# Kernel tuning notes

Measured on AMD Instinct MI355X. Metric: run time of the kernel, lower is better.

Reference implementation:

```python
import jax, jax.numpy as jnp
import numpy as np

NUM_CLASSES = 5
DIM = 512
NUM_HEADS = 8
B, N = 8, 256


def setup_inputs() -> dict:
    key = jax.random.key(0)
    ks = jax.random.split(key, 7)
    s = 1.0 / np.sqrt(DIM)
    return {
        "x": jax.random.normal(ks[0], (B, N, DIM), dtype=jnp.float32),
        "anchors": jax.random.normal(ks[1], (NUM_CLASSES, N, DIM), dtype=jnp.float32),
        "weights": jax.random.uniform(ks[2], (B, NUM_HEADS, NUM_CLASSES), dtype=jnp.float32),
        "qk_w": jax.random.normal(ks[3], (DIM, DIM), dtype=jnp.float32) * s,
        "v_w": jax.random.normal(ks[4], (DIM, DIM), dtype=jnp.float32) * s,
        "proj_w": jax.random.normal(ks[5], (DIM, DIM), dtype=jnp.float32) * s,
        "proj_b": jnp.zeros((DIM,), dtype=jnp.float32),
    }


def reference(x, anchors, weights, qk_w, v_w, proj_w, proj_b):
    Bx, Nx, C = x.shape
    H = NUM_HEADS
    hd = C // H
    scale = hd ** (-0.5)

    # v: [B, H, N, hd]
    v = (x @ v_w.T).reshape(Bx, Nx, H, hd).transpose(0, 2, 1, 3)
    # q: [B, H, N, hd]; k: [cls, H, N, hd] (shared qk projection)
    q = (x @ qk_w.T).reshape(Bx, Nx, H, hd).transpose(0, 2, 1, 3)
    k = (anchors @ qk_w.T).reshape(NUM_CLASSES, Nx, H, hd).transpose(0, 2, 1, 3)

    # a0: [B, cls, H, N, N]
    a0 = jnp.einsum("bhnd,chmd->bchnm", q, k) * scale
    left = jax.nn.relu(-a0)                         # relu of negative branch
    right = jax.nn.relu(jnp.swapaxes(a0, -2, -1))   # relu of transposed positive branch
    # second large NxN matmul, then softmax over dim=-2 (columns)
    attn = jax.nn.softmax(left @ right, axis=-2)    # [B, cls, H, N, N]

    # class-weighted combine: weights [B, H, cls] -> tmp [B, H, N, N]
    tmp = jnp.einsum("bhc,bchnm->bhnm", weights, attn)

    # (tmp @ v): [B, H, N, hd]; torch reshapes directly to (B, N, C) without permute
    out = (tmp @ v).reshape(Bx, Nx, C)
    out = out @ proj_w.T + proj_b
    return (out, a0)
```

## Files before the change

### kernel.cpp

```cpp
#include <hip/hip_runtime.h>
#include <hip/hip_fp16.h>
#include <cstdint>

#define BB 8
#define NN 256
#define NC 5
#define NH 8
#define DIM 512
#define HD 64

typedef _Float16 half_t;
typedef _Float16 h8 __attribute__((ext_vector_type(8)));
typedef _Float16 h4 __attribute__((ext_vector_type(4)));
typedef float f4 __attribute__((ext_vector_type(4)));
typedef uint32_t u4v __attribute__((ext_vector_type(4)));

__device__ __forceinline__ f4 mfma16(h8 a, h8 b, f4 c) {
  return __builtin_amdgcn_mfma_f32_16x16x32_f16(a, b, c, 0, 0, 0);
}

static __device__ const h8 HZERO = {(_Float16)0, (_Float16)0, (_Float16)0, (_Float16)0,
                                    (_Float16)0, (_Float16)0, (_Float16)0, (_Float16)0};

__device__ __forceinline__ h8 relu_pos_h8(h8 x) {
#if __has_builtin(__builtin_elementwise_max)
  return __builtin_elementwise_max(x, HZERO);
#else
  u4v u = __builtin_bit_cast(u4v, x);
  const u4v k1 = {0x00010001u, 0x00010001u, 0x00010001u, 0x00010001u};
  u4v s = (u >> 15) & k1;
  u4v m = (s << 16) - s;
  u = u & ~m;
  return __builtin_bit_cast(h8, u);
#endif
}

__device__ __forceinline__ h8 relu_neg_h8(h8 x) {
#if __has_builtin(__builtin_elementwise_max)
  return __builtin_elementwise_max(-x, HZERO);
#else
  u4v u = __builtin_bit_cast(u4v, x);
  const u4v k1 = {0x00010001u, 0x00010001u, 0x00010001u, 0x00010001u};
  const u4v ks = {0x80008000u, 0x80008000u, 0x80008000u, 0x80008000u};
  u4v s = (u >> 15) & k1;
  u4v m = (s << 16) - s;
  u = (u ^ ks) & m;
  return __builtin_bit_cast(h8, u);
#endif
}

__device__ __forceinline__ void barrier_lds() {
  __builtin_amdgcn_sched_barrier(0);
  asm volatile("s_waitcnt lgkmcnt(0)" ::: "memory");
  __builtin_amdgcn_s_barrier();
  asm volatile("" ::: "memory");
  __builtin_amdgcn_sched_barrier(0);
}

__global__ __launch_bounds__(256) void cvt_all(const float* __restrict__ x,
                                               const float* __restrict__ anchors,
                                               const float* __restrict__ qk_w,
                                               const float* __restrict__ v_w,
                                               const float* __restrict__ proj_w,
                                               half_t* __restrict__ x_h,
                                               half_t* __restrict__ anc_h,
                                               half_t* __restrict__ qk_h,
                                               half_t* __restrict__ v_wh,
                                               half_t* __restrict__ pw_h) {
  int i = blockIdx.x * 256 + threadIdx.x;
  const float* src;
  half_t* dst;
  int off;
  if (i < 262144)      { src = x;       dst = x_h;   off = i; }
  else if (i < 425984) { src = anchors; dst = anc_h; off = i - 262144; }
  else if (i < 491520) { src = qk_w;    dst = qk_h;  off = i - 425984; }
  else if (i < 557056) { src = v_w;     dst = v_wh;  off = i - 491520; }
  else                 { src = proj_w;  dst = pw_h;  off = i - 557056; }
  float4 v = ((const float4*)src)[off];
  h4 o;
  o[0] = (_Float16)v.x; o[1] = (_Float16)v.y; o[2] = (_Float16)v.z; o[3] = (_Float16)v.w;
  ((h4*)dst)[off] = o;
}

__global__ __launch_bounds__(256) void proj_all(const half_t* __restrict__ x_h,
                                                const half_t* __restrict__ anc_h,
                                                const half_t* __restrict__ qk_h,
                                                const half_t* __restrict__ v_wh,
                                                half_t* __restrict__ q_h,
                                                half_t* __restrict__ k_h,
                                                half_t* __restrict__ vT) {
  const int bx = blockIdx.x, by = blockIdx.y;
  const int tid = threadIdx.x;
  const int w = tid >> 6, lane = tid & 63;
  const int lr = lane & 15, lk = (lane >> 4) * 8, lg = lane >> 4;

  const half_t* A;
  const half_t* W;
  int mode, rt0;
  if (bx < 32)      { A = x_h;   W = qk_h; mode = 0; rt0 = bx * 64; }
  else if (bx < 52) { A = anc_h; W = qk_h; mode = 1; rt0 = (bx - 32) * 64; }
  else              { A = x_h;   W = v_wh; mode = 2; rt0 = (bx - 52) * 64; }

  const int row0 = rt0 + w * 16;
  const int col0 = by * 64;
  const f4 fz = {0.f, 0.f, 0.f, 0.f};
  f4 acc[4] = {fz, fz, fz, fz};
  const half_t* arow = A + (size_t)(row0 + lr) * DIM;

  if (mode != 2) {
    for (int k0 = 0; k0 < DIM; k0 += 32) {
      h8 a = *(const h8*)(arow + k0 + lk);
#pragma unroll
      for (int ct = 0; ct < 4; ++ct) {
        h8 b = *(const h8*)(W + (size_t)(col0 + ct * 16 + lr) * DIM + k0 + lk);
        acc[ct] = mfma16(a, b, acc[ct]);
      }
    }
    half_t* out = (mode == 0) ? q_h : k_h;
#pragma unroll
    for (int ct = 0; ct < 4; ++ct) {
      int col = col0 + ct * 16 + lr;
#pragma unroll
      for (int r = 0; r < 4; ++r) {
        int row = row0 + lg * 4 + r;
        out[(size_t)row * DIM + col] = (half_t)acc[ct][r];
      }
    }
  } else {
    for (int k0 = 0; k0 < DIM; k0 += 32) {
      h8 a = *(const h8*)(arow + k0 + lk);
#pragma unroll
      for (int ct = 0; ct < 4; ++ct) {
        h8 b = *(const h8*)(W + (size_t)(col0 + ct * 16 + lr) * DIM + k0 + lk);
        acc[ct] = mfma16(b, a, acc[ct]);
      }
    }
    const int xrow = row0 + lr;
#pragma unroll
    for (int ct = 0; ct < 4; ++ct) {
#pragma unroll
      for (int r = 0; r < 4; ++r) {
        int col = col0 + ct * 16 + lg * 4 + r;
        vT[(size_t)col * (BB * NN) + xrow] = (half_t)acc[ct][r];
      }
    }
  }
}

__global__ __launch_bounds__(1024, 4) void fused_attn5(const half_t* __restrict__ q_h,
                                                       const half_t* __restrict__ k_h,
                                                       const half_t* __restrict__ vT,
                                                       const float* __restrict__ weights,
                                                       float* __restrict__ a0_base,
                                                       half_t* __restrict__ U4) {
  extern __shared__ char smem[];
  half_t* a0s = (half_t*)smem;
  half_t* kst = (half_t*)(smem + 65536);
  half_t* vst = kst;
  half_t* wbuf = (half_t*)(smem + 98304);
  float2* scr = (float2*)(smem + 118784);
  float2* scr2 = (float2*)(smem + 135168);

  const int id = blockIdx.x;
  const int b = id / 80;
  const int rem = id % 80;
  const int c = rem / 16;
  const int h = (rem >> 1) & 7;
  const int q = rem & 1;

  const int tid = threadIdx.x;
  const int w = tid >> 6, lane = tid & 63;
  const int lr = lane & 15, lk = (lane >> 4) * 8, lg = lane >> 4;
  const int n0 = w * 16;

  const half_t* qb = q_h + (size_t)(b * NN) * DIM + h * HD;
  const half_t* kb = k_h + (size_t)(c * NN) * DIM + h * HD;
  const half_t* vTb = vT + (size_t)(h * HD) * (BB * NN) + b * NN;
  float* a0out = a0_base + (size_t)((b * NC + c) * NH + h) * (NN * NN);
  const float wgt = weights[(b * NH + h) * NC + c];

  const f4 fz = {0.f, 0.f, 0.f, 0.f};

  h8 qf0 = *(const h8*)(qb + (size_t)(n0 + lr) * DIM + lk);
  h8 qf1 = *(const h8*)(qb + (size_t)(n0 + lr) * DIM + 32 + lk);

#pragma unroll
  for (int pass = 0; pass < 2; ++pass) {
    int slot = pass * 1024 + tid;
    int row = slot >> 3, k8 = (slot & 7) * 8;
    h8 val = *(const h8*)(kb + (size_t)row * DIM + k8);
    *(h8*)(kst + ((row * 64 + k8) ^ ((row & 7) << 3))) = val;
  }
  barrier_lds();

  half_t* Lb = wbuf + w * 640;
  h8 La[8];
  const bool myhalf = ((w >> 3) == q);
  const int rl = (w & 7) * 16 + lr;
#pragma unroll
  for (int mt = 0; mt < 16; ++mt) {
    const int krow = mt * 16 + lr;
    h8 kf0 = *(const h8*)(kst + ((krow * 64 + lk) ^ ((krow & 7) << 3)));
    h8 kf1 = *(const h8*)(kst + ((krow * 64 + 32 + lk) ^ ((krow & 7) << 3)));
    f4 acc = mfma16(kf0, qf0, fz);
    acc = mfma16(kf1, qf1, acc);
    f4 v0;
    h4 hv;
#pragma unroll
    for (int r = 0; r < 4; ++r) {
      v0[r] = acc[r] * 0.125f;
      hv[r] = (_Float16)v0[r];
    }
    *(h4*)(Lb + lr * 40 + (mt & 1) * 16 + lg * 4) = hv;
    if (myhalf) {
      *(f4*)(a0out + (size_t)(n0 + lr) * NN + mt * 16 + lg * 4) = v0;
      *(h4*)(a0s + ((rl * 256 + mt * 16 + lg * 4) ^ ((rl & 7) << 3))) = hv;
    }
    if (mt & 1) {
      h8 raw = *(const h8*)(Lb + lr * 40 + lg * 8);
      La[mt >> 1] = relu_neg_h8(raw);
    }
  }
  barrier_lds();

  {
    int d = tid >> 4, m8 = (tid & 15) * 8;
    h8 val = *(const h8*)(vTb + (size_t)d * (BB * NN) + q * 128 + m8);
    *(h8*)(vst + ((d * 128 + m8) ^ ((d & 7) << 4))) = val;
  }

  f4 sacc[8];
#pragma unroll
  for (int ct = 0; ct < 8; ++ct) sacc[ct] = fz;
#pragma unroll
  for (int kc = 0; kc < 8; ++kc) {
#pragma unroll
    for (int ct = 0; ct < 8; ++ct) {
      const int rr = ct * 16 + lr;
      h8 R = relu_pos_h8(*(const h8*)(a0s + ((rr * 256 + kc * 32 + lk) ^ ((rr & 7) << 3))));
      sacc[ct] = mfma16(La[kc], R, sacc[ct]);
    }
  }

  float mw[8];
#pragma unroll
  for (int ct = 0; ct < 8; ++ct) {
    float v = 0.f;
#pragma unroll
    for (int r = 0; r < 4; ++r) v = fmaxf(v, sacc[ct][r]);
    v = fmaxf(v, __shfl_xor(v, 16, 64));
    v = fmaxf(v, __shfl_xor(v, 32, 64));
    mw[ct] = v;
    float s = 0.f;
#pragma unroll
    for (int r = 0; r < 4; ++r) {
      float e = __expf(sacc[ct][r] - v);
      sacc[ct][r] = e;
      s += e;
    }
    s += __shfl_xor(s, 16, 64);
    s += __shfl_xor(s, 32, 64);
    if (lane < 16) {
      float2 t;
      t.x = v;
      t.y = s;
      scr[w * 128 + ct * 16 + lr] = t;
    }
  }
  barrier_lds();

  if (tid < 128) {
    float gm = 0.f;
#pragma unroll
    for (int ww = 0; ww < 16; ++ww) gm = fmaxf(gm, scr[ww * 128 + tid].x);
    float sg = 0.f;
#pragma unroll
    for (int ww = 0; ww < 16; ++ww) {
      float2 t = scr[ww * 128 + tid];
      sg += t.y * __expf(t.x - gm);
    }
    float2 r;
    r.x = gm;
    r.y = sg;
    scr2[tid] = r;
  }
  barrier_lds();

  float fac[8];
#pragma unroll
  for (int ct = 0; ct < 8; ++ct) {
    float2 t = scr2[ct * 16 + lr];
    fac[ct] = __expf(mw[ct] - t.x) * wgt / t.y;
  }

  half_t* pbw = wbuf + w * 640;
  f4 uacc[4] = {fz, fz, fz, fz};
#pragma unroll
  for (int pan = 0; pan < 4; ++pan) {
#pragma unroll
    for (int ctl = 0; ctl < 2; ++ctl) {
      const int ct = pan * 2 + ctl;
      h4 hv;
#pragma unroll
      for (int r = 0; r < 4; ++r) hv[r] = (_Float16)(sacc[ct][r] * fac[ct]);
      *(h4*)(pbw + (ctl * 16 + lr) * 20 + lg * 4) = hv;
    }
    h8 pf;
#pragma unroll
    for (int e = 0; e < 8; ++e) pf[e] = pbw[(lg * 8 + e) * 20 + lr];
#pragma unroll
    for (int dt = 0; dt < 4; ++dt) {
      const int dr = dt * 16 + lr;
      h8 vf = *(const h8*)(vst + ((dr * 128 + pan * 32 + lk) ^ ((dr & 7) << 4)));
      uacc[dt] = mfma16(vf, pf, uacc[dt]);
    }
  }

  half_t* U4b = U4 + (size_t)(((b * NC + c) * NH + h) * 2 + q) * (NN * HD);
#pragma unroll
  for (int dt = 0; dt < 4; ++dt) {
    h4 hv;
#pragma unroll
    for (int r = 0; r < 4; ++r) hv[r] = (_Float16)uacc[dt][r];
    *(h4*)(U4b + (size_t)(n0 + lr) * HD + dt * 16 + lg * 4) = hv;
  }
}

__global__ __launch_bounds__(256) void reduce_u(const half_t* __restrict__ U4,
                                                half_t* __restrict__ out_head) {
  int t = blockIdx.x * 256 + threadIdx.x;
  int bh = t >> 11;
  int e = (t & 2047) * 8;
  int b = bh >> 3, h = bh & 7;
  float acc[8] = {0.f, 0.f, 0.f, 0.f, 0.f, 0.f, 0.f, 0.f};
#pragma unroll
  for (int c = 0; c < NC; ++c)
#pragma unroll
    for (int qq = 0; qq < 2; ++qq) {
      h8 u = *(const h8*)(U4 + (size_t)(((b * NC + c) * NH + h) * 2 + qq) * (NN * HD) + e);
#pragma unroll
      for (int j = 0; j < 8; ++j) acc[j] += (float)u[j];
    }
  h8 o;
#pragma unroll
  for (int j = 0; j < 8; ++j) o[j] = (_Float16)acc[j];
  *(h8*)(out_head + (size_t)bh * (NN * HD) + e) = o;
}

__global__ __launch_bounds__(256) void out_proj(const half_t* __restrict__ out_head,
                                                const half_t* __restrict__ pw_h,
                                                const float* __restrict__ pb,
                                                float* __restrict__ out0) {
  const int tid = threadIdx.x;
  const int w = tid >> 6, lane = tid & 63;
  const int lr = lane & 15, lk = (lane >> 4) * 8, lg = lane >> 4;
  const int row0 = blockIdx.x * 64 + w * 16;
  const int col0 = blockIdx.y * 64;
  const int r_ = row0 + lr;
  const int b = r_ >> 8, i = r_ & 255;
  const int hh = i >> 5;
  const f4 fz = {0.f, 0.f, 0.f, 0.f};
  f4 acc[4] = {fz, fz, fz, fz};
  for (int k0 = 0; k0 < DIM; k0 += 32) {
    const int k = k0 + lk;
    const int n = ((i & 31) << 3) | (k >> 6);
    const int d = k & 63;
    h8 a = *(const h8*)(out_head + (size_t)((b * NH + hh) * NN + n) * HD + d);
#pragma unroll
    for (int ct = 0; ct < 4; ++ct) {
      h8 bf = *(const h8*)(pw_h + (size_t)(col0 + ct * 16 + lr) * DIM + k0 + lk);
      acc[ct] = mfma16(a, bf, acc[ct]);
    }
  }
#pragma unroll
  for (int ct = 0; ct < 4; ++ct) {
    int col = col0 + ct * 16 + lr;
    float bias = pb[col];
#pragma unroll
    for (int r = 0; r < 4; ++r) {
      int row = row0 + lg * 4 + r;
      out0[(size_t)row * DIM + col] = acc[ct][r] + bias;
    }
  }
}

extern "C" void kernel_launch(void* const* d_in, const int* in_sizes, int n_in,
                              void* d_out, int out_size, void* d_ws, size_t ws_size,
                              hipStream_t stream) {
  const float* x = (const float*)d_in[0];
  const float* anchors = (const float*)d_in[1];
  const float* weights = (const float*)d_in[2];
  const float* qk_w = (const float*)d_in[3];
  const float* v_w = (const float*)d_in[4];
  const float* proj_w = (const float*)d_in[5];
  const float* proj_b = (const float*)d_in[6];

  float* out0 = (float*)d_out;
  float* a0_out = out0 + (size_t)BB * NN * DIM;

  char* ws = (char*)d_ws;
  const size_t MB = 1024 * 1024;
  half_t* x_h   = (half_t*)(ws);
  half_t* anc_h = (half_t*)(ws + 2 * MB);
  half_t* qk_h  = (half_t*)(ws + 3407872);
  half_t* v_wh  = (half_t*)(ws + 3932160);
  half_t* U4    = (half_t*)(ws);
  half_t* pw_h     = (half_t*)(ws + 20 * MB);
  half_t* q_h      = (half_t*)(ws + 20 * MB + 524288);
  half_t* k_h      = (half_t*)(ws + 22 * MB + 524288);
  half_t* vT       = (half_t*)(ws + 24 * MB);
  half_t* out_head = (half_t*)(ws + 26 * MB);

  cvt_all<<<dim3(2432), 256, 0, stream>>>(x, anchors, qk_w, v_w, proj_w,
                                          x_h, anc_h, qk_h, v_wh, pw_h);

  proj_all<<<dim3(84, 8), 256, 0, stream>>>(x_h, anc_h, qk_h, v_wh, q_h, k_h, vT);

  const size_t lds_bytes = 65536 + 32768 + 20480 + 16384 + 1024;
  fused_attn5<<<dim3(BB * NC * NH * 2), 1024, lds_bytes, stream>>>(q_h, k_h, vT, weights,
                                                                   a0_out, U4);

  reduce_u<<<dim3(512), 256, 0, stream>>>(U4, out_head);

  out_proj<<<dim3(32, 8), 256, 0, stream>>>(out_head, pw_h, proj_b, out0);

  (void)in_sizes; (void)n_in; (void)out_size; (void)ws_size;
}
```

Measured before the change: 116.0 us.

## Compute full 256x256 a0 tile per block and split second matmul 2D across waves

```diff
diff --git a/kernel.cpp b/kernel.cpp
--- a/kernel.cpp
+++ b/kernel.cpp
@@ -147,7 +147,7 @@
   }
 }
 
-__global__ __launch_bounds__(1024, 4) void fused_attn5(const half_t* __restrict__ q_h,
+__global__ __launch_bounds__(1024, 4) void fused_attn8(const half_t* __restrict__ q_h,
                                                        const half_t* __restrict__ k_h,
                                                        const half_t* __restrict__ vT,
                                                        const float* __restrict__ weights,
@@ -155,23 +155,23 @@
                                                        half_t* __restrict__ U4) {
   extern __shared__ char smem[];
   half_t* a0s = (half_t*)smem;
-  half_t* kst = (half_t*)(smem + 65536);
-  half_t* vst = kst;
-  half_t* wbuf = (half_t*)(smem + 98304);
-  float2* scr = (float2*)(smem + 118784);
-  float2* scr2 = (float2*)(smem + 135168);
+  half_t* kst = (half_t*)(smem + 98304);
+  half_t* vst = (half_t*)smem;
+  half_t* pbuf = (half_t*)(smem + 32768);
+  float2* scr = (float2*)(smem + 131072);
+  float2* scr2 = (float2*)(smem + 147456);
 
   const int id = blockIdx.x;
-  const int b = id / 80;
-  const int rem = id % 80;
-  const int c = rem / 16;
-  const int h = (rem >> 1) & 7;
-  const int q = rem & 1;
+  const int b = id / 40;
+  const int rem = id % 40;
+  const int c = rem / 8;
+  const int h = rem & 7;
 
   const int tid = threadIdx.x;
   const int w = tid >> 6, lane = tid & 63;
   const int lr = lane & 15, lk = (lane >> 4) * 8, lg = lane >> 4;
   const int n0 = w * 16;
+  const int sg = w & 7, cg = w >> 3;
 
   const half_t* qb = q_h + (size_t)(b * NN) * DIM + h * HD;
   const half_t* kb = k_h + (size_t)(c * NN) * DIM + h * HD;
@@ -193,52 +193,48 @@
   }
   barrier_lds();
 
-  half_t* Lb = wbuf + w * 640;
-  h8 La[8];
-  const bool myhalf = ((w >> 3) == q);
-  const int rl = (w & 7) * 16 + lr;
+  f4 acc[16];
 #pragma unroll
   for (int mt = 0; mt < 16; ++mt) {
     const int krow = mt * 16 + lr;
     h8 kf0 = *(const h8*)(kst + ((krow * 64 + lk) ^ ((krow & 7) << 3)));
     h8 kf1 = *(const h8*)(kst + ((krow * 64 + 32 + lk) ^ ((krow & 7) << 3)));
-    f4 acc = mfma16(kf0, qf0, fz);
-    acc = mfma16(kf1, qf1, acc);
-    f4 v0;
+    acc[mt] = mfma16(kf0, qf0, fz);
+    acc[mt] = mfma16(kf1, qf1, acc[mt]);
+#pragma unroll
+    for (int r = 0; r < 4; ++r) acc[mt][r] *= 0.125f;
+  }
+  barrier_lds();
+
+  const int na = n0 + lr;
+#pragma unroll
+  for (int mt = 0; mt < 16; ++mt) {
+    const int mb = mt * 16 + lg * 4;
     h4 hv;
 #pragma unroll
-    for (int r = 0; r < 4; ++r) {
-      v0[r] = acc[r] * 0.125f;
-      hv[r] = (_Float16)v0[r];
-    }
-    *(h4*)(Lb + lr * 40 + (mt & 1) * 16 + lg * 4) = hv;
-    if (myhalf) {
-      *(f4*)(a0out + (size_t)(n0 + lr) * NN + mt * 16 + lg * 4) = v0;
-      *(h4*)(a0s + ((rl * 256 + mt * 16 + lg * 4) ^ ((rl & 7) << 3))) = hv;
-    }
-    if (mt & 1) {
-      h8 raw = *(const h8*)(Lb + lr * 40 + lg * 8);
-      La[mt >> 1] = relu_neg_h8(raw);
-    }
+    for (int r = 0; r < 4; ++r) hv[r] = (_Float16)acc[mt][r];
+    *(h4*)(a0s + ((na * NN + mb) ^ ((na & 7) << 3))) = hv;
+    *(f4*)(a0out + (size_t)na * NN + mb) = acc[mt];
   }
   barrier_lds();
 
-  {
-    int d = tid >> 4, m8 = (tid & 15) * 8;
-    h8 val = *(const h8*)(vTb + (size_t)d * (BB * NN) + q * 128 + m8);
-    *(h8*)(vst + ((d * 128 + m8) ^ ((d & 7) << 4))) = val;
-  }
-
-  f4 sacc[8];
-#pragma unroll
-  for (int ct = 0; ct < 8; ++ct) sacc[ct] = fz;
+  f4 sacc[8][2];
+#pragma unroll
+  for (int ct = 0; ct < 8; ++ct) {
+    sacc[ct][0] = fz;
+    sacc[ct][1] = fz;
+  }
 #pragma unroll
   for (int kc = 0; kc < 8; ++kc) {
+    const int rl0 = sg * 32 + lr, rl1 = sg * 32 + 16 + lr;
+    h8 La0 = relu_neg_h8(*(const h8*)(a0s + ((rl0 * NN + kc * 32 + lk) ^ ((rl0 & 7) << 3))));
+    h8 La1 = relu_neg_h8(*(const h8*)(a0s + ((rl1 * NN + kc * 32 + lk) ^ ((rl1 & 7) << 3))));
 #pragma unroll
     for (int ct = 0; ct < 8; ++ct) {
-      const int rr = ct * 16 + lr;
-      h8 R = relu_pos_h8(*(const h8*)(a0s + ((rr * 256 + kc * 32 + lk) ^ ((rr & 7) << 3))));
-      sacc[ct] = mfma16(La[kc], R, sacc[ct]);
+      const int rr = cg * 128 + ct * 16 + lr;
+      h8 R = relu_pos_h8(*(const h8*)(a0s + ((rr * NN + kc * 32 + lk) ^ ((rr & 7) << 3))));
+      sacc[ct][0] = mfma16(La0, R, sacc[ct][0]);
+      sacc[ct][1] = mfma16(La1, R, sacc[ct][1]);
     }
   }
 
@@ -247,83 +243,112 @@
   for (int ct = 0; ct < 8; ++ct) {
     float v = 0.f;
 #pragma unroll
-    for (int r = 0; r < 4; ++r) v = fmaxf(v, sacc[ct][r]);
+    for (int rt = 0; rt < 2; ++rt)
+#pragma unroll
+      for (int r = 0; r < 4; ++r) v = fmaxf(v, sacc[ct][rt][r]);
     v = fmaxf(v, __shfl_xor(v, 16, 64));
     v = fmaxf(v, __shfl_xor(v, 32, 64));
     mw[ct] = v;
     float s = 0.f;
 #pragma unroll
-    for (int r = 0; r < 4; ++r) {
-      float e = __expf(sacc[ct][r] - v);
-      sacc[ct][r] = e;
-      s += e;
-    }
+    for (int rt = 0; rt < 2; ++rt)
+#pragma unroll
+      for (int r = 0; r < 4; ++r) {
+        float e = __expf(sacc[ct][rt][r] - v);
+        sacc[ct][rt][r] = e;
+        s += e;
+      }
     s += __shfl_xor(s, 16, 64);
     s += __shfl_xor(s, 32, 64);
     if (lane < 16) {
       float2 t;
       t.x = v;
       t.y = s;
-      scr[w * 128 + ct * 16 + lr] = t;
+      scr[sg * 256 + cg * 128 + ct * 16 + lr] = t;
     }
   }
   barrier_lds();
 
-  if (tid < 128) {
+  if (tid < 256) {
     float gm = 0.f;
 #pragma unroll
-    for (int ww = 0; ww < 16; ++ww) gm = fmaxf(gm, scr[ww * 128 + tid].x);
-    float sg = 0.f;
-#pragma unroll
-    for (int ww = 0; ww < 16; ++ww) {
-      float2 t = scr[ww * 128 + tid];
-      sg += t.y * __expf(t.x - gm);
+    for (int ww = 0; ww < 8; ++ww) gm = fmaxf(gm, scr[ww * 256 + tid].x);
+    float sg2 = 0.f;
+#pragma unroll
+    for (int ww = 0; ww < 8; ++ww) {
+      float2 t = scr[ww * 256 + tid];
+      sg2 += t.y * __expf(t.x - gm);
     }
     float2 r;
     r.x = gm;
-    r.y = sg;
+    r.y = sg2;
     scr2[tid] = r;
   }
+#pragma unroll
+  for (int pass = 0; pass < 2; ++pass) {
+    int slot = pass * 1024 + tid;
+    int d = slot >> 5, m8 = (slot & 31) * 8;
+    h8 vv = *(const h8*)(vTb + (size_t)d * (BB * NN) + m8);
+    *(h8*)(vst + ((d * NN + m8) ^ ((d & 7) << 3))) = vv;
+  }
   barrier_lds();
 
-  float fac[8];
 #pragma unroll
   for (int ct = 0; ct < 8; ++ct) {
-    float2 t = scr2[ct * 16 + lr];
-    fac[ct] = __expf(mw[ct] - t.x) * wgt / t.y;
-  }
-
-  half_t* pbw = wbuf + w * 640;
-  f4 uacc[4] = {fz, fz, fz, fz};
-#pragma unroll
-  for (int pan = 0; pan < 4; ++pan) {
+    float2 t = scr2[cg * 128 + ct * 16 + lr];
+    float fac = __expf(mw[ct] - t.x) * wgt / t.y;
+#pragma unroll
+    for (int rt = 0; rt < 2; ++rt)
+#pragma unroll
+      for (int r = 0; r < 4; ++r) sacc[ct][rt][r] *= fac;
+  }
+
+  half_t* pbw = pbuf + w * 1344;
+  f4 uacc[4][2];
+#pragma unroll
+  for (int dt = 0; dt < 4; ++dt) {
+    uacc[dt][0] = fz;
+    uacc[dt][1] = fz;
+  }
+#pragma unroll
+  for (int p = 0; p < 4; ++p) {
 #pragma unroll
     for (int ctl = 0; ctl < 2; ++ctl) {
-      const int ct = pan * 2 + ctl;
-      h4 hv;
-#pragma unroll
-      for (int r = 0; r < 4; ++r) hv[r] = (_Float16)(sacc[ct][r] * fac[ct]);
-      *(h4*)(pbw + (ctl * 16 + lr) * 20 + lg * 4) = hv;
-    }
-    h8 pf;
-#pragma unroll
-    for (int e = 0; e < 8; ++e) pf[e] = pbw[(lg * 8 + e) * 20 + lr];
+      const int ct = p * 2 + ctl;
+#pragma unroll
+      for (int rt = 0; rt < 2; ++rt) {
+        h4 hv;
+#pragma unroll
+        for (int r = 0; r < 4; ++r) hv[r] = (_Float16)sacc[ct][rt][r];
+        *(h4*)(pbw + (ctl * 16 + lr) * 42 + rt * 16 + lg * 4) = hv;
+      }
+    }
+    h8 pf0, pf1;
+#pragma unroll
+    for (int e = 0; e < 8; ++e) {
+      pf0[e] = pbw[(lg * 8 + e) * 42 + lr];
+      pf1[e] = pbw[(lg * 8 + e) * 42 + 16 + lr];
+    }
 #pragma unroll
     for (int dt = 0; dt < 4; ++dt) {
       const int dr = dt * 16 + lr;
-      h8 vf = *(const h8*)(vst + ((dr * 128 + pan * 32 + lk) ^ ((dr & 7) << 4)));
-      uacc[dt] = mfma16(vf, pf, uacc[dt]);
-    }
-  }
-
-  half_t* U4b = U4 + (size_t)(((b * NC + c) * NH + h) * 2 + q) * (NN * HD);
-#pragma unroll
-  for (int dt = 0; dt < 4; ++dt) {
-    h4 hv;
-#pragma unroll
-    for (int r = 0; r < 4; ++r) hv[r] = (_Float16)uacc[dt][r];
-    *(h4*)(U4b + (size_t)(n0 + lr) * HD + dt * 16 + lg * 4) = hv;
-  }
+      h8 vf = *(const h8*)(vst + ((dr * NN + cg * 128 + p * 32 + lg * 8) ^ ((dr & 7) << 3)));
+      uacc[dt][0] = mfma16(vf, pf0, uacc[dt][0]);
+      uacc[dt][1] = mfma16(vf, pf1, uacc[dt][1]);
+    }
+  }
+
+  half_t* U4b = U4 + (size_t)(((b * NC + c) * NH + h) * 2 + cg) * (NN * HD);
+#pragma unroll
+  for (int dt = 0; dt < 4; ++dt)
+#pragma unroll
+    for (int nt = 0; nt < 2; ++nt) {
+      int n = sg * 32 + nt * 16 + lr;
+      h4 hv;
+#pragma unroll
+      for (int r = 0; r < 4; ++r) hv[r] = (_Float16)uacc[dt][nt][r];
+      *(h4*)(U4b + (size_t)n * HD + dt * 16 + lg * 4) = hv;
+    }
 }
 
 __global__ __launch_bounds__(256) void reduce_u(const half_t* __restrict__ U4,
@@ -416,9 +441,9 @@
 
   proj_all<<<dim3(84, 8), 256, 0, stream>>>(x_h, anc_h, qk_h, v_wh, q_h, k_h, vT);
 
-  const size_t lds_bytes = 65536 + 32768 + 20480 + 16384 + 1024;
-  fused_attn5<<<dim3(BB * NC * NH * 2), 1024, lds_bytes, stream>>>(q_h, k_h, vT, weights,
-                                                                   a0_out, U4);
+  const size_t lds_bytes = 131072 + 16384 + 2048;
+  fused_attn8<<<dim3(BB * NC * NH), 1024, lds_bytes, stream>>>(q_h, k_h, vT, weights,
+                                                               a0_out, U4);
 
   reduce_u<<<dim3(512), 256, 0, stream>>>(U4, out_head);
 
```

Result: slower. 126.5 us (+9.0%).

## Split attention into 1280 smaller blocks with per-block partial U outputs

Applied to the files above, without the earlier changes.

```diff
diff --git a/kernel.cpp b/kernel.cpp
--- a/kernel.cpp
+++ b/kernel.cpp
@@ -147,6 +147,227 @@
   }
 }
 
+__global__ __launch_bounds__(512, 4) void fused_attn9(const half_t* __restrict__ q_h,
+                                                      const half_t* __restrict__ k_h,
+                                                      const half_t* __restrict__ vT,
+                                                      const float* __restrict__ weights,
+                                                      float* __restrict__ a0_base,
+                                                      half_t* __restrict__ U16) {
+  extern __shared__ char smem[];
+  half_t* kst = (half_t*)smem;
+  half_t* a0s = (half_t*)(smem + 32768);
+  half_t* lbuf = (half_t*)(smem + 65536);
+  float2* scr = (float2*)smem;
+  float2* scr2 = (float2*)(smem + 4096);
+  half_t* pbuf = (half_t*)(smem + 4608);
+
+  const int bid = blockIdx.x;
+  const int task = bid >> 2, qt = bid & 3;
+  const int b = task / 40;
+  const int rem = task % 40;
+  const int c = rem / 8;
+  const int h = rem & 7;
+
+  const int tid = threadIdx.x;
+  const int w = tid >> 6, lane = tid & 63;
+  const int lr = lane & 15, lk = (lane >> 4) * 8, lg = lane >> 4;
+
+  const half_t* qb = q_h + (size_t)(b * NN) * DIM + h * HD;
+  const half_t* kb = k_h + (size_t)(c * NN) * DIM + h * HD;
+  const half_t* vTb = vT + (size_t)(h * HD) * (BB * NN) + b * NN;
+  float* a0out = a0_base + (size_t)((b * NC + c) * NH + h) * (NN * NN);
+  const float wgt = weights[(b * NH + h) * NC + c];
+  const f4 fz = {0.f, 0.f, 0.f, 0.f};
+
+#pragma unroll
+  for (int pass = 0; pass < 4; ++pass) {
+    int slot = pass * 512 + tid;
+    int row = slot >> 3, k8 = (slot & 7) * 8;
+    *(h8*)(kst + ((row * 64 + k8) ^ ((row & 7) << 3))) =
+        *(const h8*)(kb + (size_t)row * DIM + k8);
+  }
+  barrier_lds();
+
+  half_t* Lb = lbuf + w * 640;
+  h8 La[2][8];
+  const bool own = ((w >> 1) == qt);
+#pragma unroll
+  for (int p = 0; p < 2; ++p) {
+    const int nbase = w * 32 + p * 16;
+    h8 qf0 = *(const h8*)(qb + (size_t)(nbase + lr) * DIM + lk);
+    h8 qf1 = *(const h8*)(qb + (size_t)(nbase + lr) * DIM + 32 + lk);
+    const int row_l = (w & 1) * 32 + p * 16 + lr;
+#pragma unroll
+    for (int mt = 0; mt < 16; ++mt) {
+      const int krow = mt * 16 + lr;
+      h8 kf0 = *(const h8*)(kst + ((krow * 64 + lk) ^ ((krow & 7) << 3)));
+      h8 kf1 = *(const h8*)(kst + ((krow * 64 + 32 + lk) ^ ((krow & 7) << 3)));
+      f4 acc = mfma16(kf0, qf0, fz);
+      acc = mfma16(kf1, qf1, acc);
+      f4 v0;
+      h4 hv;
+#pragma unroll
+      for (int r = 0; r < 4; ++r) {
+        v0[r] = acc[r] * 0.125f;
+        hv[r] = (_Float16)v0[r];
+      }
+      *(h4*)(Lb + lr * 40 + (mt & 1) * 16 + lg * 4) = hv;
+      if (own) {
+        *(f4*)(a0out + (size_t)(nbase + lr) * NN + mt * 16 + lg * 4) = v0;
+        *(h4*)(a0s + ((row_l * NN + mt * 16 + lg * 4) ^ ((row_l & 7) << 3))) = hv;
+      }
+      if (mt & 1) {
+        h8 raw = *(const h8*)(Lb + lr * 40 + lg * 8);
+        La[p][mt >> 1] = relu_neg_h8(raw);
+      }
+    }
+  }
+  barrier_lds();
+
+  f4 sacc[4][2];
+#pragma unroll
+  for (int ct = 0; ct < 4; ++ct) {
+    sacc[ct][0] = fz;
+    sacc[ct][1] = fz;
+  }
+#pragma unroll
+  for (int kc = 0; kc < 8; ++kc) {
+#pragma unroll
+    for (int ct = 0; ct < 4; ++ct) {
+      const int rr = ct * 16 + lr;
+      h8 R = relu_pos_h8(*(const h8*)(a0s + ((rr * NN + kc * 32 + lk) ^ ((rr & 7) << 3))));
+      sacc[ct][0] = mfma16(La[0][kc], R, sacc[ct][0]);
+      sacc[ct][1] = mfma16(La[1][kc], R, sacc[ct][1]);
+    }
+  }
+
+  float mw[4];
+#pragma unroll
+  for (int ct = 0; ct < 4; ++ct) {
+    float v = 0.f;
+#pragma unroll
+    for (int rt = 0; rt < 2; ++rt)
+#pragma unroll
+      for (int r = 0; r < 4; ++r) v = fmaxf(v, sacc[ct][rt][r]);
+    v = fmaxf(v, __shfl_xor(v, 16, 64));
+    v = fmaxf(v, __shfl_xor(v, 32, 64));
+    mw[ct] = v;
+    float s = 0.f;
+#pragma unroll
+    for (int rt = 0; rt < 2; ++rt)
+#pragma unroll
+      for (int r = 0; r < 4; ++r) {
+        float e = __expf(sacc[ct][rt][r] - v);
+        sacc[ct][rt][r] = e;
+        s += e;
+      }
+    s += __shfl_xor(s, 16, 64);
+    s += __shfl_xor(s, 32, 64);
+    if (lane < 16) {
+      float2 t;
+      t.x = v;
+      t.y = s;
+      scr[w * 64 + ct * 16 + lr] = t;
+    }
+  }
+  barrier_lds();
+
+  if (tid < 64) {
+    float gm = 0.f;
+    float sg = 0.f;
+    float2 t[8];
+#pragma unroll
+    for (int ww = 0; ww < 8; ++ww) {
+      t[ww] = scr[ww * 64 + tid];
+      gm = fmaxf(gm, t[ww].x);
+    }
+#pragma unroll
+    for (int ww = 0; ww < 8; ++ww) sg += t[ww].y * __expf(t[ww].x - gm);
+    float2 r;
+    r.x = gm;
+    r.y = sg;
+    scr2[tid] = r;
+  }
+  barrier_lds();
+
+#pragma unroll
+  for (int ct = 0; ct < 4; ++ct) {
+    float2 t = scr2[ct * 16 + lr];
+    float fac = __expf(mw[ct] - t.x) * wgt / t.y;
+#pragma unroll
+    for (int rt = 0; rt < 2; ++rt)
+#pragma unroll
+      for (int r = 0; r < 4; ++r) sacc[ct][rt][r] *= fac;
+  }
+
+  half_t* pbw = pbuf + w * 1152;
+  f4 uacc[4][2];
+#pragma unroll
+  for (int dt = 0; dt < 4; ++dt) {
+    uacc[dt][0] = fz;
+    uacc[dt][1] = fz;
+  }
+#pragma unroll
+  for (int p2 = 0; p2 < 2; ++p2) {
+#pragma unroll
+    for (int ctl = 0; ctl < 2; ++ctl) {
+      const int ct = p2 * 2 + ctl;
+#pragma unroll
+      for (int rt = 0; rt < 2; ++rt) {
+        h4 hv;
+#pragma unroll
+        for (int r = 0; r < 4; ++r) hv[r] = (_Float16)sacc[ct][rt][r];
+        *(h4*)(pbw + (ctl * 16 + lr) * 36 + rt * 16 + lg * 4) = hv;
+      }
+    }
+    h8 pf0, pf1;
+#pragma unroll
+    for (int e = 0; e < 8; ++e) {
+      pf0[e] = pbw[(lg * 8 + e) * 36 + lr];
+      pf1[e] = pbw[(lg * 8 + e) * 36 + 16 + lr];
+    }
+#pragma unroll
+    for (int dt = 0; dt < 4; ++dt) {
+      h8 vf = *(const h8*)(vTb + (size_t)(dt * 16 + lr) * (BB * NN) + qt * 64 + p2 * 32 + lg * 8);
+      uacc[dt][0] = mfma16(vf, pf0, uacc[dt][0]);
+      uacc[dt][1] = mfma16(vf, pf1, uacc[dt][1]);
+    }
+  }
+
+  half_t* Ub = U16 + (size_t)(task * 4 + qt) * (NN * HD);
+#pragma unroll
+  for (int dt = 0; dt < 4; ++dt)
+#pragma unroll
+    for (int nt = 0; nt < 2; ++nt) {
+      int n = w * 32 + nt * 16 + lr;
+      h4 hv;
+#pragma unroll
+      for (int r = 0; r < 4; ++r) hv[r] = (_Float16)uacc[dt][nt][r];
+      *(h4*)(Ub + (size_t)n * HD + dt * 16 + lg * 4) = hv;
+    }
+}
+
+__global__ __launch_bounds__(256) void reduce_u20(const half_t* __restrict__ U16,
+                                                  half_t* __restrict__ out_head) {
+  int t = blockIdx.x * 256 + threadIdx.x;
+  int bh = t >> 11;
+  int e = (t & 2047) * 8;
+  int b = bh >> 3, h = bh & 7;
+  float acc[8] = {0.f, 0.f, 0.f, 0.f, 0.f, 0.f, 0.f, 0.f};
+#pragma unroll
+  for (int c = 0; c < NC; ++c)
+#pragma unroll
+    for (int qq = 0; qq < 4; ++qq) {
+      h8 u = *(const h8*)(U16 + (size_t)(((b * NC + c) * NH + h) * 4 + qq) * (NN * HD) + e);
+#pragma unroll
+      for (int j = 0; j < 8; ++j) acc[j] += (float)u[j];
+    }
+  h8 o;
+#pragma unroll
+  for (int j = 0; j < 8; ++j) o[j] = (_Float16)acc[j];
+  *(h8*)(out_head + (size_t)bh * (NN * HD) + e) = o;
+}
+
 __global__ __launch_bounds__(1024, 4) void fused_attn5(const half_t* __restrict__ q_h,
                                                        const half_t* __restrict__ k_h,
                                                        const half_t* __restrict__ vT,
@@ -400,29 +621,58 @@
 
   char* ws = (char*)d_ws;
   const size_t MB = 1024 * 1024;
-  half_t* x_h   = (half_t*)(ws);
-  half_t* anc_h = (half_t*)(ws + 2 * MB);
-  half_t* qk_h  = (half_t*)(ws + 3407872);
-  half_t* v_wh  = (half_t*)(ws + 3932160);
-  half_t* U4    = (half_t*)(ws);
-  half_t* pw_h     = (half_t*)(ws + 20 * MB);
-  half_t* q_h      = (half_t*)(ws + 20 * MB + 524288);
-  half_t* k_h      = (half_t*)(ws + 22 * MB + 524288);
-  half_t* vT       = (half_t*)(ws + 24 * MB);
-  half_t* out_head = (half_t*)(ws + 26 * MB);
-
-  cvt_all<<<dim3(2432), 256, 0, stream>>>(x, anchors, qk_w, v_w, proj_w,
-                                          x_h, anc_h, qk_h, v_wh, pw_h);
-
-  proj_all<<<dim3(84, 8), 256, 0, stream>>>(x_h, anc_h, qk_h, v_wh, q_h, k_h, vT);
-
-  const size_t lds_bytes = 65536 + 32768 + 20480 + 16384 + 1024;
-  fused_attn5<<<dim3(BB * NC * NH * 2), 1024, lds_bytes, stream>>>(q_h, k_h, vT, weights,
-                                                                   a0_out, U4);
-
-  reduce_u<<<dim3(512), 256, 0, stream>>>(U4, out_head);
-
-  out_proj<<<dim3(32, 8), 256, 0, stream>>>(out_head, pw_h, proj_b, out0);
-
-  (void)in_sizes; (void)n_in; (void)out_size; (void)ws_size;
-}
+
+  const size_t A_U16 = 0;
+  const size_t A_pw = (size_t)1280 * NN * HD * 2;
+  const size_t A_q = A_pw + 524288;
+  const size_t A_k = A_q + 2097152;
+  const size_t A_vT = A_k + 1310720;
+  const size_t A_oh = A_vT + 2097152;
+  const size_t A_need = A_oh + 2097152;
+
+  if (ws_size >= A_need) {
+    half_t* x_h   = (half_t*)(ws);
+    half_t* anc_h = (half_t*)(ws + 2 * MB);
+    half_t* qk_h  = (half_t*)(ws + 3407872);
+    half_t* v_wh  = (half_t*)(ws + 3932160);
+    half_t* U16   = (half_t*)(ws + A_U16);
+    half_t* pw_h  = (half_t*)(ws + A_pw);
+    half_t* q_h   = (half_t*)(ws + A_q);
+    half_t* k_h   = (half_t*)(ws + A_k);
+    half_t* vT    = (half_t*)(ws + A_vT);
+    half_t* out_head = (half_t*)(ws + A_oh);
+
+    cvt_all<<<dim3(2432), 256, 0, stream>>>(x, anchors, qk_w, v_w, proj_w,
+                                            x_h, anc_h, qk_h, v_wh, pw_h);
+    proj_all<<<dim3(84, 8), 256, 0, stream>>>(x_h, anc_h, qk_h, v_wh, q_h, k_h, vT);
+
+    const size_t lds9 = 32768 + 32768 + 10240;
+    fused_attn9<<<dim3(BB * NC * NH * 4), 512, lds9, stream>>>(q_h, k_h, vT, weights,
+                                                               a0_out, U16);
+    reduce_u20<<<dim3(512), 256, 0, stream>>>(U16, out_head);
+    out_proj<<<dim3(32, 8), 256, 0, stream>>>(out_head, pw_h, proj_b, out0);
+  } else {
+    half_t* x_h   = (half_t*)(ws);
+    half_t* anc_h = (half_t*)(ws + 2 * MB);
+    half_t* qk_h  = (half_t*)(ws + 3407872);
+    half_t* v_wh  = (half_t*)(ws + 3932160);
+    half_t* U4    = (half_t*)(ws);
+    half_t* pw_h     = (half_t*)(ws + 20 * MB);
+    half_t* q_h      = (half_t*)(ws + 20 * MB + 524288);
+    half_t* k_h      = (half_t*)(ws + 22 * MB + 524288);
+    half_t* vT       = (half_t*)(ws + 24 * MB);
+    half_t* out_head = (half_t*)(ws + 26 * MB);
+
+    cvt_all<<<dim3(2432), 256, 0, stream>>>(x, anchors, qk_w, v_w, proj_w,
+                                            x_h, anc_h, qk_h, v_wh, pw_h);
+    proj_all<<<dim3(84, 8), 256, 0, stream>>>(x_h, anc_h, qk_h, v_wh, q_h, k_h, vT);
+
+    const size_t lds5 = 65536 + 32768 + 20480 + 16384 + 1024;
+    fused_attn5<<<dim3(BB * NC * NH * 2), 1024, lds5, stream>>>(q_h, k_h, vT, weights,
+                                                                a0_out, U4);
+    reduce_u<<<dim3(512), 256, 0, stream>>>(U4, out_head);
+    out_proj<<<dim3(32, 8), 256, 0, stream>>>(out_head, pw_h, proj_b, out0);
+  }
+
+  (void)in_sizes; (void)n_in; (void)out_size;
+}
```

New measurement: 150.9 us. 30.0% more time.

## Fuse class/partial reduction of U4 into output projection kernel

Applied to the files above, without the earlier changes.

```diff
diff --git a/kernel.cpp b/kernel.cpp
--- a/kernel.cpp
+++ b/kernel.cpp
@@ -326,61 +326,71 @@
   }
 }
 
-__global__ __launch_bounds__(256) void reduce_u(const half_t* __restrict__ U4,
-                                                half_t* __restrict__ out_head) {
-  int t = blockIdx.x * 256 + threadIdx.x;
-  int bh = t >> 11;
-  int e = (t & 2047) * 8;
-  int b = bh >> 3, h = bh & 7;
-  float acc[8] = {0.f, 0.f, 0.f, 0.f, 0.f, 0.f, 0.f, 0.f};
-#pragma unroll
-  for (int c = 0; c < NC; ++c)
-#pragma unroll
-    for (int qq = 0; qq < 2; ++qq) {
-      h8 u = *(const h8*)(U4 + (size_t)(((b * NC + c) * NH + h) * 2 + qq) * (NN * HD) + e);
-#pragma unroll
-      for (int j = 0; j < 8; ++j) acc[j] += (float)u[j];
-    }
-  h8 o;
-#pragma unroll
-  for (int j = 0; j < 8; ++j) o[j] = (_Float16)acc[j];
-  *(h8*)(out_head + (size_t)bh * (NN * HD) + e) = o;
-}
-
-__global__ __launch_bounds__(256) void out_proj(const half_t* __restrict__ out_head,
-                                                const half_t* __restrict__ pw_h,
-                                                const float* __restrict__ pb,
-                                                float* __restrict__ out0) {
+__global__ __launch_bounds__(256) void out_projA(const half_t* __restrict__ U4,
+                                                 const half_t* __restrict__ pw_h,
+                                                 const float* __restrict__ pb,
+                                                 float* __restrict__ out0) {
+  __shared__ half_t Ast[32 * 520];
+  const int bid = blockIdx.x;
+  const int b = bid >> 3, hh = bid & 7;
   const int tid = threadIdx.x;
+
+  {
+    const int il = tid >> 3, kk = tid & 7;
+    const int n = (il << 3) | kk;
+    const half_t* base = U4 + ((size_t)(b * NC * NH + hh) * 2) * (NN * HD) + (size_t)n * HD;
+#pragma unroll
+    for (int d0 = 0; d0 < HD; d0 += 8) {
+      float a8[8] = {0.f, 0.f, 0.f, 0.f, 0.f, 0.f, 0.f, 0.f};
+#pragma unroll
+      for (int cc = 0; cc < NC; ++cc)
+#pragma unroll
+        for (int qq = 0; qq < 2; ++qq) {
+          h8 u = *(const h8*)(base + (size_t)(cc * NH * 2 + qq) * (NN * HD) + d0);
+#pragma unroll
+          for (int j = 0; j < 8; ++j) a8[j] += (float)u[j];
+        }
+      h8 o;
+#pragma unroll
+      for (int j = 0; j < 8; ++j) o[j] = (_Float16)a8[j];
+      *(h8*)(&Ast[il * 520 + kk * 64 + d0]) = o;
+    }
+  }
+  __syncthreads();
+
   const int w = tid >> 6, lane = tid & 63;
   const int lr = lane & 15, lk = (lane >> 4) * 8, lg = lane >> 4;
-  const int row0 = blockIdx.x * 64 + w * 16;
-  const int col0 = blockIdx.y * 64;
-  const int r_ = row0 + lr;
-  const int b = r_ >> 8, i = r_ & 255;
-  const int hh = i >> 5;
+  const int col0 = w * 128;
   const f4 fz = {0.f, 0.f, 0.f, 0.f};
-  f4 acc[4] = {fz, fz, fz, fz};
-  for (int k0 = 0; k0 < DIM; k0 += 32) {
-    const int k = k0 + lk;
-    const int n = ((i & 31) << 3) | (k >> 6);
-    const int d = k & 63;
-    h8 a = *(const h8*)(out_head + (size_t)((b * NH + hh) * NN + n) * HD + d);
-#pragma unroll
-    for (int ct = 0; ct < 4; ++ct) {
-      h8 bf = *(const h8*)(pw_h + (size_t)(col0 + ct * 16 + lr) * DIM + k0 + lk);
-      acc[ct] = mfma16(a, bf, acc[ct]);
-    }
-  }
-#pragma unroll
-  for (int ct = 0; ct < 4; ++ct) {
+  f4 acc[2][8];
+#pragma unroll
+  for (int rt = 0; rt < 2; ++rt)
+#pragma unroll
+    for (int ct = 0; ct < 8; ++ct) acc[rt][ct] = fz;
+
+  for (int kc = 0; kc < 16; ++kc) {
+    h8 a0f = *(const h8*)(&Ast[(lr)*520 + kc * 32 + lk]);
+    h8 a1f = *(const h8*)(&Ast[(16 + lr) * 520 + kc * 32 + lk]);
+#pragma unroll
+    for (int ct = 0; ct < 8; ++ct) {
+      h8 bf = *(const h8*)(pw_h + (size_t)(col0 + ct * 16 + lr) * DIM + kc * 32 + lk);
+      acc[0][ct] = mfma16(a0f, bf, acc[0][ct]);
+      acc[1][ct] = mfma16(a1f, bf, acc[1][ct]);
+    }
+  }
+
+  const int row_base = b * NN + hh * 32;
+#pragma unroll
+  for (int ct = 0; ct < 8; ++ct) {
     int col = col0 + ct * 16 + lr;
     float bias = pb[col];
 #pragma unroll
-    for (int r = 0; r < 4; ++r) {
-      int row = row0 + lg * 4 + r;
-      out0[(size_t)row * DIM + col] = acc[ct][r] + bias;
-    }
+    for (int rt = 0; rt < 2; ++rt)
+#pragma unroll
+      for (int r = 0; r < 4; ++r) {
+        int row = row_base + rt * 16 + lg * 4 + r;
+        out0[(size_t)row * DIM + col] = acc[rt][ct][r] + bias;
+      }
   }
 }
 
@@ -405,24 +415,21 @@
   half_t* qk_h  = (half_t*)(ws + 3407872);
   half_t* v_wh  = (half_t*)(ws + 3932160);
   half_t* U4    = (half_t*)(ws);
-  half_t* pw_h     = (half_t*)(ws + 20 * MB);
-  half_t* q_h      = (half_t*)(ws + 20 * MB + 524288);
-  half_t* k_h      = (half_t*)(ws + 22 * MB + 524288);
-  half_t* vT       = (half_t*)(ws + 24 * MB);
-  half_t* out_head = (half_t*)(ws + 26 * MB);
+  half_t* pw_h = (half_t*)(ws + 20 * MB);
+  half_t* q_h  = (half_t*)(ws + 20 * MB + 524288);
+  half_t* k_h  = (half_t*)(ws + 22 * MB + 524288);
+  half_t* vT   = (half_t*)(ws + 24 * MB);
 
   cvt_all<<<dim3(2432), 256, 0, stream>>>(x, anchors, qk_w, v_w, proj_w,
                                           x_h, anc_h, qk_h, v_wh, pw_h);
 
   proj_all<<<dim3(84, 8), 256, 0, stream>>>(x_h, anc_h, qk_h, v_wh, q_h, k_h, vT);
 
-  const size_t lds_bytes = 65536 + 32768 + 20480 + 16384 + 1024;
-  fused_attn5<<<dim3(BB * NC * NH * 2), 1024, lds_bytes, stream>>>(q_h, k_h, vT, weights,
-                                                                   a0_out, U4);
-
-  reduce_u<<<dim3(512), 256, 0, stream>>>(U4, out_head);
-
-  out_proj<<<dim3(32, 8), 256, 0, stream>>>(out_head, pw_h, proj_b, out0);
+  const size_t lds5 = 65536 + 32768 + 20480 + 16384 + 1024;
+  fused_attn5<<<dim3(BB * NC * NH * 2), 1024, lds5, stream>>>(q_h, k_h, vT, weights,
+                                                              a0_out, U4);
+
+  out_projA<<<dim3(64), 256, 0, stream>>>(U4, pw_h, proj_b, out0);
 
   (void)in_sizes; (void)n_in; (void)out_size; (void)ws_size;
 }
```

Result: slower. 143.7 us (+23.8%).
